# Kernel tuning notes

Measured on AMD Instinct MI355X. Metric: run time of the kernel, lower is better.

The kernel has to match this reference:

```python
import jax, jax.numpy as jnp
import numpy as np

# Compartment limits: name -> (start, size) along the locus axis of X
LIMITS = {"cortex_L": (0, 29696), "cortex_R": (29696, 29716)}
N_LOCI = 59412
T = 500
N_ENC = 200  # encodings per compartment


def setup_inputs() -> dict:
    key = jax.random.key(0)
    kx, kl, kr = jax.random.split(key, 3)
    X = jax.random.normal(kx, (N_LOCI, T), dtype=jnp.float32)
    W_L = jax.random.normal(kl, (N_ENC, LIMITS["cortex_L"][1]), dtype=jnp.float32)
    W_R = jax.random.normal(kr, (N_ENC, LIMITS["cortex_R"][1]), dtype=jnp.float32)
    return {"X": X, "W_L": W_L, "W_R": W_R}


def _compartmentalised_linear(X, weights):
    # Apply each compartment's weight matrix to its index-range slice of X.
    refs = []
    for name, W in weights.items():
        start, size = LIMITS[name]
        refs.append(W @ jax.lax.dynamic_slice_in_dim(X, start, size, axis=0))
    return jnp.concatenate(refs, axis=0)  # [sum(n_enc), T]


def _pairedcorr(A, B):
    # Pearson correlation between every row of A and every row of B (over time).
    Ac = A - A.mean(axis=-1, keepdims=True)
    Bc = B - B.mean(axis=-1, keepdims=True)
    num = Ac @ Bc.T  # [n_ref, n_loci]
    denom = jnp.linalg.norm(Ac, axis=-1)[:, None] * jnp.linalg.norm(Bc, axis=-1)[None, :]
    return num / denom


def reference(X, W_L, W_R):
    references = _compartmentalised_linear(X, {"cortex_L": W_L, "cortex_R": W_R})  # [400, T]
    return _pairedcorr(references, X)  # [400, N_LOCI]
```

## Files before the change

### kernel.cpp

```cpp
#include <hip/hip_runtime.h>

typedef __attribute__((ext_vector_type(8))) __bf16 bf16x8;
typedef __attribute__((ext_vector_type(8))) unsigned short u16x8;
typedef __attribute__((ext_vector_type(4))) unsigned short u16x4;
typedef __attribute__((ext_vector_type(4))) float f32x4;

#define N_LOCI   59412
#define T_DIM    500
#define T_PAD    512
#define N_ENC    200
#define KL       29696
#define KR       29716
#define J_PAD    59648
#define G1_S     58

__device__ __forceinline__ unsigned short cvt1(float x) {
    __bf16 h = (__bf16)x;
    return __builtin_bit_cast(unsigned short, h);
}
__device__ __forceinline__ float bf2f(unsigned short h) {
    return __uint_as_float(((unsigned)h) << 16);
}
__device__ __forceinline__ f32x4 mfma16(u16x8 a, u16x8 b, f32x4 c) {
    return __builtin_amdgcn_mfma_f32_16x16x32_bf16(
        __builtin_bit_cast(bf16x8, a), __builtin_bit_cast(bf16x8, b), c, 0, 0, 0);
}

__global__ __launch_bounds__(256) void k0_xraw(const float* __restrict__ X,
                                               unsigned short* __restrict__ Xb,
                                               float2* __restrict__ xstat) {
    const int w    = threadIdx.x >> 6;
    const int lane = threadIdx.x & 63;
    const int base = blockIdx.x * 16 + w * 4;
    for (int i = 0; i < 4; ++i) {
        const int row = base + i;
        unsigned short* out = Xb + (size_t)row * T_PAD;
        if (row >= N_LOCI) {
            u16x4 z = {0, 0, 0, 0};
            *(u16x4*)(out + lane * 4) = z;
            *(u16x4*)(out + (lane + 64) * 4) = z;
            if (lane == 0) xstat[row] = make_float2(0.0f, 0.0f);
            continue;
        }
        const float4* xr = (const float4*)(X + (size_t)row * T_DIM);
        float4 v1 = xr[lane];
        float4 v2 = make_float4(0.f, 0.f, 0.f, 0.f);
        const bool has2 = (lane + 64) < 125;
        if (has2) v2 = xr[lane + 64];
        float s = v1.x + v1.y + v1.z + v1.w + v2.x + v2.y + v2.z + v2.w;
        float q = v1.x * v1.x + v1.y * v1.y + v1.z * v1.z + v1.w * v1.w
                + v2.x * v2.x + v2.y * v2.y + v2.z * v2.z + v2.w * v2.w;
        #pragma unroll
        for (int off = 32; off; off >>= 1) {
            s += __shfl_xor(s, off);
            q += __shfl_xor(q, off);
        }
        u16x4 w1, w2 = {0, 0, 0, 0};
        w1[0] = cvt1(v1.x); w1[1] = cvt1(v1.y); w1[2] = cvt1(v1.z); w1[3] = cvt1(v1.w);
        if (has2) {
            w2[0] = cvt1(v2.x); w2[1] = cvt1(v2.y); w2[2] = cvt1(v2.z); w2[3] = cvt1(v2.w);
        }
        *(u16x4*)(out + lane * 4) = w1;
        *(u16x4*)(out + (lane + 64) * 4) = w2;
        if (lane == 0) {
            const float mu = s * (1.0f / 500.0f);
            xstat[row] = make_float2(mu, rsqrtf(q - 500.0f * mu * mu));
        }
    }
}

__global__ __launch_bounds__(256) void k2_gemm1(const unsigned short* __restrict__ Xb,
                                                const float* __restrict__ WL,
                                                const float* __restrict__ WR,
                                                unsigned short* __restrict__ P16) {
    const int d = blockIdx.x;
    const int g = d & 127;
    if (g >= 2 * G1_S) return;
    const int slot = d >> 7;
    const int mt = slot >> 2;
    const int nt = slot & 3;
    const int sc   = g >> 1;
    const int comp = g & 1;
    const int K      = comp ? KR : KL;
    const float* W   = comp ? WR : WL;
    const int xbase  = comp ? KL : 0;
    const int m0 = mt * 128;
    const int n0 = nt * 128;

    __shared__ unsigned short As[128 * 64];
    __shared__ unsigned short Bs[128 * 64];

    const int t = threadIdx.x, lane = t & 63, wid = t >> 6;
    const int wm = wid >> 1, wn = wid & 1;
    const int lr = lane & 15, lg = lane >> 4;

    f32x4 acc[4][4];
    #pragma unroll
    for (int i = 0; i < 4; ++i)
        #pragma unroll
        for (int j = 0; j < 4; ++j) {
            f32x4 z = {0.f, 0.f, 0.f, 0.f};
            acc[i][j] = z;
        }

    const int nsteps = (comp && sc == G1_S - 1) ? 9 : 8;

    const int am = t >> 1, aseg = t & 1;
    const int arow = (m0 + am < N_ENC) ? (m0 + am) : (N_ENC - 1);
    const float* wrow = W + (size_t)arow * K;
    const int akey = (am & 7) << 3;
    const int kq = t >> 4, tc = t & 15;

    u16x8 ha[4];
    u16x8 hb4[4];

    auto load_tiles = [&](int st) {
        const int k0 = sc * 512 + st * 64;
        {
            const int kb = k0 + aseg * 32;
            float av[32];
            if (kb + 31 < K) {
                #pragma unroll
                for (int f = 0; f < 8; ++f) {
                    const float4 v = *(const float4*)(wrow + kb + f * 4);
                    av[f * 4 + 0] = v.x; av[f * 4 + 1] = v.y;
                    av[f * 4 + 2] = v.z; av[f * 4 + 3] = v.w;
                }
            } else {
                #pragma unroll
                for (int j = 0; j < 32; ++j)
                    av[j] = (kb + j < K) ? wrow[kb + j] : 0.0f;
            }
            #pragma unroll
            for (int q = 0; q < 4; ++q) {
                u16x8 hh;
                #pragma unroll
                for (int j = 0; j < 8; ++j) hh[j] = cvt1(av[q * 8 + j]);
                ha[q] = hh;
            }
        }
        #pragma unroll
        for (int r = 0; r < 4; ++r) {
            const int krel = k0 + kq * 4 + r;
            if (krel < K) {
                hb4[r] = *(const u16x8*)(Xb + (size_t)(xbase + krel) * T_PAD + n0 + tc * 8);
            } else {
                u16x8 z = {0, 0, 0, 0, 0, 0, 0, 0};
                hb4[r] = z;
            }
        }
    };

    auto write_stage = [&]() {
        #pragma unroll
        for (int q = 0; q < 4; ++q)
            *(u16x8*)&As[am * 64 + ((aseg * 32 + q * 8) ^ akey)] = ha[q];
        #pragma unroll
        for (int j = 0; j < 8; ++j) {
            const int nl = tc * 8 + j;
            const int key = ((nl ^ (nl >> 3)) & 7) << 3;
            u16x4 w4 = { hb4[0][j], hb4[1][j], hb4[2][j], hb4[3][j] };
            *(u16x4*)&Bs[nl * 64 + ((kq * 4) ^ key)] = w4;
        }
    };

    load_tiles(0);
    for (int st = 0; st < nsteps; ++st) {
        write_stage();
        __syncthreads();
        if (st + 1 < nsteps) load_tiles(st + 1);
        #pragma unroll
        for (int h = 0; h < 2; ++h) {
            u16x8 af[4], bf[4];
            #pragma unroll
            for (int mf = 0; mf < 4; ++mf) {
                const int m = wm * 64 + mf * 16 + lr;
                af[mf] = *(const u16x8*)&As[m * 64 + ((h * 32 + lg * 8) ^ ((m & 7) << 3))];
            }
            #pragma unroll
            for (int nf = 0; nf < 4; ++nf) {
                const int nl = wn * 64 + nf * 16 + lr;
                const int key = ((nl ^ (nl >> 3)) & 7) << 3;
                bf[nf] = *(const u16x8*)&Bs[nl * 64 + ((h * 32 + lg * 8) ^ key)];
            }
            #pragma unroll
            for (int mf = 0; mf < 4; ++mf)
                #pragma unroll
                for (int nf = 0; nf < 4; ++nf)
                    acc[mf][nf] = mfma16(af[mf], bf[nf], acc[mf][nf]);
        }
        __syncthreads();
    }

    unsigned short* Pb = P16 + (size_t)g * (200 * 512);
    #pragma unroll
    for (int mf = 0; mf < 4; ++mf)
        #pragma unroll
        for (int rr = 0; rr < 4; ++rr) {
            const int m = m0 + wm * 64 + mf * 16 + lg * 4 + rr;
            if (m < N_ENC) {
                #pragma unroll
                for (int nf = 0; nf < 4; ++nf) {
                    const int n = n0 + wn * 64 + nf * 16 + lr;
                    Pb[(size_t)m * 512 + n] = cvt1(acc[mf][nf][rr]);
                }
            }
        }
}

__global__ __launch_bounds__(256) void k3_astats(const unsigned short* __restrict__ P16,
                                                 unsigned short* __restrict__ Ab,
                                                 float2* __restrict__ astat) {
    const int r = blockIdx.x;
    const int t = threadIdx.x;
    unsigned short* out = Ab + (size_t)r * T_PAD;
    if (r >= 2 * N_ENC) {
        out[t] = 0; out[t + 256] = 0;
        if (t == 0) astat[r] = make_float2(0.0f, 0.0f);
        return;
    }
    const int comp = (r >= N_ENC) ? 1 : 0;
    const int m = r - comp * N_ENC;
    float a1 = 0.0f, a2 = 0.0f;
    for (int s2 = 0; s2 < G1_S; ++s2) {
        const unsigned short* Pb = P16 + ((size_t)(s2 * 2 + comp) * 200 + m) * 512;
        a1 += bf2f(Pb[t]);
        a2 += bf2f(Pb[t + 256]);
    }
    const bool v2ok = (t + 256) < T_DIM;
    const float b2 = v2ok ? a2 : 0.0f;
    float s = a1 + b2;
    float q = a1 * a1 + b2 * b2;
    #pragma unroll
    for (int off = 32; off; off >>= 1) {
        s += __shfl_xor(s, off);
        q += __shfl_xor(q, off);
    }
    __shared__ float ls[4], lq[4];
    if ((t & 63) == 0) { ls[t >> 6] = s; lq[t >> 6] = q; }
    __syncthreads();
    const float S = ls[0] + ls[1] + ls[2] + ls[3];
    const float Q = lq[0] + lq[1] + lq[2] + lq[3];
    const float mean = S * (1.0f / 500.0f);
    const float iv   = rsqrtf(Q - 500.0f * mean * mean);
    out[t] = cvt1(a1);
    out[t + 256] = v2ok ? cvt1(a2) : (unsigned short)0;
    if (t == 0) astat[r] = make_float2(mean, iv);
}

__global__ __launch_bounds__(256, 3) void k4_gemm2(const unsigned short* __restrict__ Ab,
                                                   const unsigned short* __restrict__ Xb,
                                                   const float2* __restrict__ astat,
                                                   const float2* __restrict__ xstat,
                                                   float* __restrict__ C) {
    const int d  = blockIdx.x;
    const int jt = (d >> 5) * 8 + (d & 7);
    if (jt >= 465) return;
    const int mt = (d >> 3) & 3;
    const int j0 = jt * 128;
    const int m0 = mt * 128;

    __shared__ unsigned short As[128 * 64];
    __shared__ unsigned short Bs[128 * 64];
    const int t = threadIdx.x, lane = t & 63;
    const int wm = (t >> 6) >> 1, wnn = (t >> 6) & 1;
    const int lg = lane >> 4, lr = lane & 15;

    f32x4 acc[4][4];
    #pragma unroll
    for (int i = 0; i < 4; ++i)
        #pragma unroll
        for (int j = 0; j < 4; ++j) {
            f32x4 z = {0.f, 0.f, 0.f, 0.f};
            acc[i][j] = z;
        }

    const int ar = t >> 1, aseg = t & 1;
    const unsigned short* ag = Ab + (size_t)(m0 + ar) * T_PAD + aseg * 32;
    const unsigned short* bg = Xb + (size_t)(j0 + ar) * T_PAD + aseg * 32;
    const int akey = (ar & 7) << 3;

    u16x8 ha[4], hb[4];
    auto load4 = [&](int k0, u16x8 (&la)[4], u16x8 (&lb)[4]) {
        #pragma unroll
        for (int q = 0; q < 4; ++q) la[q] = *(const u16x8*)(ag + k0 + q * 8);
        #pragma unroll
        for (int q = 0; q < 4; ++q) lb[q] = *(const u16x8*)(bg + k0 + q * 8);
    };
    load4(0, ha, hb);

    for (int st = 0; st < 8; ++st) {
        #pragma unroll
        for (int q = 0; q < 4; ++q) {
            const int off = ar * 64 + ((aseg * 32 + q * 8) ^ akey);
            *(u16x8*)&As[off] = ha[q];
            *(u16x8*)&Bs[off] = hb[q];
        }
        __syncthreads();
        u16x8 na[4], nb[4];
        const bool more = st < 7;
        if (more) load4((st + 1) * 64, na, nb);
        #pragma unroll
        for (int h = 0; h < 2; ++h) {
            u16x8 bf4[4];
            #pragma unroll
            for (int nf = 0; nf < 4; ++nf) {
                const int n = wnn * 64 + nf * 16 + lr;
                bf4[nf] = *(const u16x8*)&Bs[n * 64 + ((h * 32 + lg * 8) ^ ((n & 7) << 3))];
            }
            #pragma unroll
            for (int mf = 0; mf < 4; ++mf) {
                const int m = wm * 64 + mf * 16 + lr;
                const u16x8 af = *(const u16x8*)&As[m * 64 + ((h * 32 + lg * 8) ^ ((m & 7) << 3))];
                #pragma unroll
                for (int nf = 0; nf < 4; ++nf)
                    acc[mf][nf] = mfma16(af, bf4[nf], acc[mf][nf]);
            }
        }
        __syncthreads();
        if (more) {
            #pragma unroll
            for (int q = 0; q < 4; ++q) { ha[q] = na[q]; hb[q] = nb[q]; }
        }
    }

    #pragma unroll
    for (int mf = 0; mf < 4; ++mf) {
        const int row = m0 + wm * 64 + mf * 16 + lg * 4;
        #pragma unroll
        for (int nf = 0; nf < 4; ++nf) {
            const int col = j0 + wnn * 64 + nf * 16 + lr;
            if (col < N_LOCI) {
                const float2 xs = xstat[col];
                #pragma unroll
                for (int rr = 0; rr < 4; ++rr) {
                    if (row + rr < 2 * N_ENC) {
                        const float2 as = astat[row + rr];
                        C[(size_t)(row + rr) * N_LOCI + col] =
                            (acc[mf][nf][rr] - 500.0f * as.x * xs.x) * as.y * xs.y;
                    }
                }
            }
        }
    }
}

extern "C" void kernel_launch(void* const* d_in, const int* in_sizes, int n_in,
                              void* d_out, int out_size, void* d_ws, size_t ws_size,
                              hipStream_t stream) {
    const float* X  = (const float*)d_in[0];
    const float* WL = (const float*)d_in[1];
    const float* WR = (const float*)d_in[2];
    float* C = (float*)d_out;

    char* w = (char*)d_ws;
    unsigned short* Xb  = (unsigned short*)w;  w += (size_t)J_PAD * T_PAD * 2;
    unsigned short* P16 = (unsigned short*)w;  w += (size_t)2 * G1_S * 200 * 512 * 2;
    unsigned short* Ab  = (unsigned short*)w;  w += (size_t)512 * 512 * 2;
    float2* astat = (float2*)w;                w += (size_t)512 * 8;
    float2* xstat = (float2*)w;

    k0_xraw<<<dim3(J_PAD / 16), dim3(256), 0, stream>>>(X, Xb, xstat);
    k2_gemm1<<<dim3(1024), dim3(256), 0, stream>>>(Xb, WL, WR, P16);
    k3_astats<<<dim3(512), dim3(256), 0, stream>>>(P16, Ab, astat);
    k4_gemm2<<<dim3(1888), dim3(256), 0, stream>>>(Ab, Xb, astat, xstat, C);
}
```

Before: 169.3 us.

## Drop LDS staging in correlation GEMM and load MFMA fragments directly from global

Replaces the shared-memory tiled, register-prefetched main loop of the second GEMM with direct per-wave global loads of A and B fragments feeding MFMA, with no LDS and no barriers. This removes LDS write/read traffic and __syncthreads stalls, relying on L1/L2 to serve the operand reuse between waves. It also drops the occupancy hint from the launch bounds. The risk is that each wave now fetches 16-byte strided rows from global memory, so the loop becomes more latency-bound without software prefetch.

```diff
diff --git a/kernel.cpp b/kernel.cpp
--- a/kernel.cpp
+++ b/kernel.cpp
@@ -248,11 +248,11 @@
     if (t == 0) astat[r] = make_float2(mean, iv);
 }
 
-__global__ __launch_bounds__(256, 3) void k4_gemm2(const unsigned short* __restrict__ Ab,
-                                                   const unsigned short* __restrict__ Xb,
-                                                   const float2* __restrict__ astat,
-                                                   const float2* __restrict__ xstat,
-                                                   float* __restrict__ C) {
+__global__ __launch_bounds__(256) void k4_gemm2(const unsigned short* __restrict__ Ab,
+                                                const unsigned short* __restrict__ Xb,
+                                                const float2* __restrict__ astat,
+                                                const float2* __restrict__ xstat,
+                                                float* __restrict__ C) {
     const int d  = blockIdx.x;
     const int jt = (d >> 5) * 8 + (d & 7);
     if (jt >= 465) return;
@@ -260,10 +260,8 @@
     const int j0 = jt * 128;
     const int m0 = mt * 128;
 
-    __shared__ unsigned short As[128 * 64];
-    __shared__ unsigned short Bs[128 * 64];
-    const int t = threadIdx.x, lane = t & 63;
-    const int wm = (t >> 6) >> 1, wnn = (t >> 6) & 1;
+    const int t = threadIdx.x, lane = t & 63, wid = t >> 6;
+    const int wm = wid >> 1, wn = wid & 1;
     const int lg = lane >> 4, lr = lane & 15;
 
     f32x4 acc[4][4];
@@ -275,53 +273,27 @@
             acc[i][j] = z;
         }
 
-    const int ar = t >> 1, aseg = t & 1;
-    const unsigned short* ag = Ab + (size_t)(m0 + ar) * T_PAD + aseg * 32;
-    const unsigned short* bg = Xb + (size_t)(j0 + ar) * T_PAD + aseg * 32;
-    const int akey = (ar & 7) << 3;
-
-    u16x8 ha[4], hb[4];
-    auto load4 = [&](int k0, u16x8 (&la)[4], u16x8 (&lb)[4]) {
-        #pragma unroll
-        for (int q = 0; q < 4; ++q) la[q] = *(const u16x8*)(ag + k0 + q * 8);
-        #pragma unroll
-        for (int q = 0; q < 4; ++q) lb[q] = *(const u16x8*)(bg + k0 + q * 8);
-    };
-    load4(0, ha, hb);
-
-    for (int st = 0; st < 8; ++st) {
-        #pragma unroll
-        for (int q = 0; q < 4; ++q) {
-            const int off = ar * 64 + ((aseg * 32 + q * 8) ^ akey);
-            *(u16x8*)&As[off] = ha[q];
-            *(u16x8*)&Bs[off] = hb[q];
-        }
-        __syncthreads();
-        u16x8 na[4], nb[4];
-        const bool more = st < 7;
-        if (more) load4((st + 1) * 64, na, nb);
-        #pragma unroll
-        for (int h = 0; h < 2; ++h) {
-            u16x8 bf4[4];
-            #pragma unroll
-            for (int nf = 0; nf < 4; ++nf) {
-                const int n = wnn * 64 + nf * 16 + lr;
-                bf4[nf] = *(const u16x8*)&Bs[n * 64 + ((h * 32 + lg * 8) ^ ((n & 7) << 3))];
-            }
-            #pragma unroll
-            for (int mf = 0; mf < 4; ++mf) {
-                const int m = wm * 64 + mf * 16 + lr;
-                const u16x8 af = *(const u16x8*)&As[m * 64 + ((h * 32 + lg * 8) ^ ((m & 7) << 3))];
-                #pragma unroll
-                for (int nf = 0; nf < 4; ++nf)
-                    acc[mf][nf] = mfma16(af, bf4[nf], acc[mf][nf]);
-            }
-        }
-        __syncthreads();
-        if (more) {
-            #pragma unroll
-            for (int q = 0; q < 4; ++q) { ha[q] = na[q]; hb[q] = nb[q]; }
-        }
+    const unsigned short* ap[4];
+    const unsigned short* bp[4];
+    #pragma unroll
+    for (int mf = 0; mf < 4; ++mf)
+        ap[mf] = Ab + (size_t)(m0 + wm * 64 + mf * 16 + lr) * T_PAD + lg * 8;
+    #pragma unroll
+    for (int nf = 0; nf < 4; ++nf)
+        bp[nf] = Xb + (size_t)(j0 + wn * 64 + nf * 16 + lr) * T_PAD + lg * 8;
+
+    #pragma unroll 2
+    for (int k0 = 0; k0 < 512; k0 += 32) {
+        u16x8 af[4], bf[4];
+        #pragma unroll
+        for (int mf = 0; mf < 4; ++mf) af[mf] = *(const u16x8*)(ap[mf] + k0);
+        #pragma unroll
+        for (int nf = 0; nf < 4; ++nf) bf[nf] = *(const u16x8*)(bp[nf] + k0);
+        #pragma unroll
+        for (int mf = 0; mf < 4; ++mf)
+            #pragma unroll
+            for (int nf = 0; nf < 4; ++nf)
+                acc[mf][nf] = mfma16(af[mf], bf[nf], acc[mf][nf]);
     }
 
     #pragma unroll
@@ -329,7 +301,7 @@
         const int row = m0 + wm * 64 + mf * 16 + lg * 4;
         #pragma unroll
         for (int nf = 0; nf < 4; ++nf) {
-            const int col = j0 + wnn * 64 + nf * 16 + lr;
+            const int col = j0 + wn * 64 + nf * 16 + lr;
             if (col < N_LOCI) {
                 const float2 xs = xstat[col];
                 #pragma unroll
```

New measurement: 249.2 us. 47.2% more time.
